# Kernel optimization log

Hardware: AMD Instinct MI355X
Metric: run time of the kernel (lower is better)

The kernel has to match this reference:

```python
import jax, jax.numpy as jnp
import numpy as np

B, L, HS, WS = 4, 5, 32, 32
C = 256            # dim == heads * dim_head
M, D = 8, 32       # heads, dim_head
T, R = 2, 4        # num_types, num_relations
I = M * D          # inner_dim
EPS = 1e-5


def setup_inputs() -> dict:
    key = jax.random.key(0)
    ks = jax.random.split(key, 12)
    w = 0.02
    x = jax.random.normal(ks[0], (B, L, HS, WS, C), dtype=jnp.float32)
    mask = jnp.ones((B, HS, WS, L, L), dtype=jnp.int32)
    prior_encoding = jax.random.randint(ks[1], (B, L, HS, WS, 3), 0, T).astype(jnp.float32)
    return {
        "x": x,
        "mask": mask,
        "prior_encoding": prior_encoding,
        "ln_w": jnp.ones((C,), jnp.float32),
        "ln_b": jnp.zeros((C,), jnp.float32),
        "Wq": jax.random.normal(ks[2], (T, C, I), jnp.float32) * w,
        "bq": jnp.zeros((T, I), jnp.float32),
        "Wk": jax.random.normal(ks[3], (T, C, I), jnp.float32) * w,
        "bk": jnp.zeros((T, I), jnp.float32),
        "Wv": jax.random.normal(ks[4], (T, C, I), jnp.float32) * w,
        "bv": jnp.zeros((T, I), jnp.float32),
        "Wa": jax.random.normal(ks[5], (T, I, C), jnp.float32) * w,
        "ba": jnp.zeros((T, C), jnp.float32),
        "rel_att": jax.random.normal(ks[6], (R, M, D, D), jnp.float32) * w,
        "rel_msg": jax.random.normal(ks[7], (R, M, D, D), jnp.float32) * w,
    }


def _hgt_forward(x, mask, prior_encoding, ln_w, ln_b, Wq, bq, Wk, bk, Wv, bv, Wa, ba, rel_att, rel_msg):
    # pre-LayerNorm over channel dim
    mu = jnp.mean(x, axis=-1, keepdims=True)
    var = jnp.mean(jnp.square(x - mu), axis=-1, keepdims=True)
    xn = (x - mu) * jax.lax.rsqrt(var + EPS) * ln_w + ln_b

    # [B,L,H,W,C] -> [B,H,W,L,C]
    xp = jnp.transpose(xn, (0, 2, 3, 1, 4))
    types = prior_encoding[:, :, 0, 0, 2].astype(jnp.int32)  # [B,L]

    # per-type q/k/v projections via gather of type-indexed weights
    q = jnp.einsum('bhwlc,blci->bhwli', xp, Wq[types]) + bq[types][:, None, None]
    k = jnp.einsum('bhwlc,blci->bhwli', xp, Wk[types]) + bk[types][:, None, None]
    v = jnp.einsum('bhwlc,blci->bhwli', xp, Wv[types]) + bv[types][:, None, None]

    def to_heads(t):  # [B,H,W,L,I] -> [B,M,H,W,L,D]
        return jnp.transpose(t.reshape(B, HS, WS, L, M, D), (0, 4, 1, 2, 3, 5))
    q, k, v = to_heads(q), to_heads(k), to_heads(v)

    # relation-indexed edge weights: e_type = t_i * T + t_j
    e = types[:, :, None] * T + types[:, None, :]              # [B,L,L]
    w_att = jnp.transpose(rel_att[e], (0, 3, 1, 2, 4, 5))      # [B,M,L,L,D,D]
    w_msg = jnp.transpose(rel_msg[e], (0, 3, 1, 2, 4, 5))

    scale = D ** -0.5
    q_w = jnp.einsum('bmhwip,bmijpq->bmhwijq', q, w_att)
    att = jnp.einsum('bmhwijq,bmhwjq->bmhwij', q_w, k) * scale
    att = jnp.where(mask[:, None] == 0, -1e9, att)
    att = jax.nn.softmax(att, axis=-1)

    v_msg = jnp.einsum('bmijpc,bmhwjp->bmhwijc', w_msg, v)
    out = jnp.einsum('bmhwij,bmhwijc->bmhwic', att, v_msg)

    # [B,M,H,W,L,D] -> [B,H,W,L,C]
    out = jnp.transpose(out, (0, 2, 3, 4, 1, 5)).reshape(B, HS, WS, L, I)
    out = jnp.einsum('bhwli,blic->bhwlc', out, Wa[types]) + ba[types][:, None, None]
    # dropout is identity at inference
    return jnp.transpose(out, (0, 3, 1, 2, 4))                 # [B,L,H,W,C]


def reference(x, mask, prior_encoding, ln_w, ln_b, Wq, bq, Wk, bk, Wv, bv, Wa, ba, rel_att, rel_msg):
    return _hgt_forward(x, mask, prior_encoding, ln_w, ln_b, Wq, bq, Wk, bk, Wv, bv, Wa, ba, rel_att, rel_msg)
```

## Files before the change

### kernel.cpp

```cpp
#include <hip/hip_runtime.h>
#include <hip/hip_bf16.h>
#include <math.h>

#define BB 4
#define LL 5
#define HSZ 32
#define WSZ 32
#define PP (HSZ*WSZ)
#define CC 256
#define MM 8
#define DD 32
#define II 256
#define TT 2
#define NTOK (BB*PP*LL*II)
#define TILE_ELEMS 8192
#define SCALE 0.17677669529663687f

typedef short bf16x8 __attribute__((ext_vector_type(8)));
typedef float f32x4 __attribute__((ext_vector_type(4)));

static __device__ __forceinline__ ushort f2bf(float f) {
    unsigned u = __float_as_uint(f);
    unsigned r = (u + 0x7fffu + ((u >> 16) & 1u)) >> 16;
    return (ushort)r;
}
static __device__ __forceinline__ float bf2f(ushort u) {
    return __uint_as_float(((unsigned)u) << 16);
}

__global__ __launch_bounds__(256) void k_fold(
    const float* __restrict__ Wq, const float* __restrict__ Wv,
    const float* __restrict__ Wk, const float* __restrict__ Wa,
    const float* __restrict__ bq, const float* __restrict__ bv,
    const float* __restrict__ rel_att, const float* __restrict__ rel_msg,
    const float* __restrict__ x,
    const float* __restrict__ lnw, const float* __restrict__ lnb,
    ushort* __restrict__ packW, float* __restrict__ bEff,
    ushort* __restrict__ xnPack)
{
    __shared__ float As[1024];
    __shared__ ushort Apack[8192];
    const int blk = blockIdx.x;
    const int tid = threadIdx.x;

    if (blk < 64) {
        const int p  = blk >> 5;
        const int t  = (blk >> 4) & 1;
        const int ts = (blk >> 3) & 1;
        const int m  = blk & 7;
        const float* A = (p == 0)
            ? rel_att + (size_t)((t * 2 + ts) * 8 + m) * 1024
            : rel_msg + (size_t)((ts * 2 + t) * 8 + m) * 1024;
        for (int i = tid; i < 1024; i += 256) As[i] = A[i];
        __syncthreads();

        const float* W = ((p == 0) ? Wq : Wv) + (size_t)t * 65536;
        const int k = tid;
        float wrow[32];
        #pragma unroll
        for (int u = 0; u < 8; ++u)
            *(float4*)&wrow[u * 4] = *(const float4*)&W[k * 256 + m * 32 + u * 4];

        const int slot = (p == 0 ? 0 : 4) + t * 2 + ts;
        ushort* base = packW + (size_t)slot * 65536;
        const int kt = k >> 5, j = k & 7, lq = ((k >> 3) & 3) * 16;
        #pragma unroll
        for (int q = 0; q < 32; ++q) {
            float acc = 0.f;
            #pragma unroll
            for (int pp = 0; pp < 32; ++pp) acc += wrow[pp] * As[pp * 32 + q];
            const int nt = m * 2 + (q >> 4);
            const int lane = lq + (q & 15);
            base[(size_t)((nt * 8 + kt) * 64 + lane) * 8 + j] = f2bf(acc);
        }
        if (tid < 32) {
            const int q = tid;
            const float* bi = ((p == 0) ? bq : bv) + t * 256 + m * 32;
            float acc = 0.f;
            #pragma unroll
            for (int pp = 0; pp < 32; ++pp) acc += bi[pp] * As[pp * 32 + q];
            bEff[(p ? 1024 : 0) + (t * 2 + ts) * 256 + m * 32 + q] = acc;
        }
    } else if (blk < 192) {
        const int idx = blk - 64;
        const int which = idx >> 6;
        const int gi = (idx & 63) * 256 + tid;
        const int t = gi >> 13;
        const int sub = gi & 8191;
        const float* src = ((which == 0) ? Wk : Wa) + (size_t)t * 65536;
        const int slot = (which == 0 ? 8 : 10) + t;
        const int nt = sub >> 9, kt = (sub >> 6) & 7, lane = sub & 63;
        const int k0 = kt * 32 + (lane >> 4) * 8;
        const int n  = nt * 16 + (lane & 15);
        ushort h[8];
        #pragma unroll
        for (int j = 0; j < 8; ++j) h[j] = f2bf(src[(size_t)(k0 + j) * 256 + n]);
        uint4 o;
        o.x = (unsigned)h[0] | ((unsigned)h[1] << 16);
        o.y = (unsigned)h[2] | ((unsigned)h[3] << 16);
        o.z = (unsigned)h[4] | ((unsigned)h[5] << 16);
        o.w = (unsigned)h[6] | ((unsigned)h[7] << 16);
        *(uint4*)(packW + (size_t)slot * 65536 + (size_t)sub * 8) = o;
    } else {
        const int lblk = blk - 192;
        const int bl  = lblk >> 5;
        const int pt  = lblk & 31;
        const int p0  = pt * 32;

        const int r  = tid >> 3;
        const int jj = tid & 7;
        const float* xrow = x + ((size_t)bl * PP + p0 + r) * CC;
        float4 xv[8];
        float s1 = 0.f, s2 = 0.f;
        #pragma unroll
        for (int u = 0; u < 8; ++u) {
            xv[u] = *(const float4*)(xrow + jj * 32 + u * 4);
            s1 += xv[u].x + xv[u].y + xv[u].z + xv[u].w;
            s2 += xv[u].x * xv[u].x + xv[u].y * xv[u].y + xv[u].z * xv[u].z + xv[u].w * xv[u].w;
        }
        s1 += __shfl_xor(s1, 1); s1 += __shfl_xor(s1, 2); s1 += __shfl_xor(s1, 4);
        s2 += __shfl_xor(s2, 1); s2 += __shfl_xor(s2, 2); s2 += __shfl_xor(s2, 4);
        const float mu   = s1 * (1.0f / 256.0f);
        const float var  = s2 * (1.0f / 256.0f) - mu * mu;
        const float rstd = rsqrtf(var + 1e-5f);

        const int mt_r = r >> 4, rm = r & 15;
        #pragma unroll
        for (int u = 0; u < 8; ++u) {
            const int c0 = jj * 32 + u * 4;
            const float4 g  = *(const float4*)(lnw + c0);
            const float4 bt = *(const float4*)(lnb + c0);
            const ushort h0 = f2bf((xv[u].x - mu) * rstd * g.x + bt.x);
            const ushort h1 = f2bf((xv[u].y - mu) * rstd * g.y + bt.y);
            const ushort h2 = f2bf((xv[u].z - mu) * rstd * g.z + bt.z);
            const ushort h3 = f2bf((xv[u].w - mu) * rstd * g.w + bt.w);
            uint2 w2;
            w2.x = (unsigned)h0 | ((unsigned)h1 << 16);
            w2.y = (unsigned)h2 | ((unsigned)h3 << 16);
            const int kt   = c0 >> 5;
            const int lsub = rm + (((c0 >> 3) & 3) << 4);
            const int j0   = c0 & 7;
            *(uint2*)&Apack[(((mt_r * 8 + kt) * 64 + lsub) << 3) + j0] = w2;
        }
        __syncthreads();

        const size_t tbase = (size_t)lblk * TILE_ELEMS;
        #pragma unroll
        for (int u = 0; u < 4; ++u) {
            const int ch = (tid + u * 256) * 8;
            *(uint4*)&xnPack[tbase + ch] = *(const uint4*)&Apack[ch];
        }
    }
}

__global__ __launch_bounds__(256) void k_proj(
    const ushort* __restrict__ xnPack, const float* __restrict__ prior,
    const ushort* __restrict__ packW, const float* __restrict__ bEff,
    const float* __restrict__ bk,
    ushort* __restrict__ qw0, ushort* __restrict__ qw1, ushort* __restrict__ kkO,
    ushort* __restrict__ vm0, ushort* __restrict__ vm1)
{
    __shared__ ushort As[8192];

    const int tid  = threadIdx.x;
    const int blk  = blockIdx.x;
    const int mat  = blk / 640;
    const int rem  = blk - mat * 640;
    const int bl   = rem >> 5;
    const int sub  = rem & 31;
    const int pg   = sub >> 1;
    const int half = sub & 1;
    const int t    = (int)prior[(size_t)bl * (PP * 3) + 2];

    int slot; const float* bias;
    if (mat < 2)       { slot = t * 2 + mat;           bias = bEff + slot * 256; }
    else if (mat == 2) { slot = 8 + t;                 bias = bk + t * 256; }
    else               { slot = 4 + t * 2 + (mat - 3); bias = bEff + 1024 + (t * 2 + (mat - 3)) * 256; }
    ushort* dst = (mat == 0) ? qw0 : (mat == 1) ? qw1 : (mat == 2) ? kkO : (mat == 3) ? vm0 : vm1;

    const int wv = tid >> 6, lane = tid & 63;

    const ushort* Bp = packW + (size_t)slot * 65536;
    bf16x8 bfr[8][2];
    #pragma unroll
    for (int kt = 0; kt < 8; ++kt)
        #pragma unroll
        for (int nn = 0; nn < 2; ++nn) {
            const int ntg = half * 8 + wv * 2 + nn;
            bfr[kt][nn] = *(const bf16x8*)&Bp[(size_t)((ntg * 8 + kt) * 64 + lane) * 8];
        }

    const int cl = lane & 15, rq = lane >> 4;
    const int colA = half * 128 + wv * 32 + cl;
    const int colB = colA + 16;
    const float biasA = bias[colA], biasB = bias[colB];

    #pragma unroll 1
    for (int tl = 0; tl < 2; ++tl) {
        const int pt = pg * 2 + tl;
        const size_t tbase = (size_t)(bl * 32 + pt) * TILE_ELEMS;
        __syncthreads();
        #pragma unroll
        for (int u = 0; u < 4; ++u) {
            const int ch = (tid + u * 256) * 8;
            *(uint4*)&As[ch] = *(const uint4*)&xnPack[tbase + ch];
        }
        __syncthreads();

        f32x4 acc[2][2];
        #pragma unroll
        for (int mt = 0; mt < 2; ++mt)
            #pragma unroll
            for (int nn = 0; nn < 2; ++nn)
                acc[mt][nn] = (f32x4){0.f, 0.f, 0.f, 0.f};

        #pragma unroll
        for (int kt = 0; kt < 8; ++kt) {
            const bf16x8 a0 = *(const bf16x8*)&As[((0 * 8 + kt) * 64 + lane) << 3];
            const bf16x8 a1 = *(const bf16x8*)&As[((1 * 8 + kt) * 64 + lane) << 3];
            acc[0][0] = __builtin_amdgcn_mfma_f32_16x16x32_bf16(a0, bfr[kt][0], acc[0][0], 0, 0, 0);
            acc[0][1] = __builtin_amdgcn_mfma_f32_16x16x32_bf16(a0, bfr[kt][1], acc[0][1], 0, 0, 0);
            acc[1][0] = __builtin_amdgcn_mfma_f32_16x16x32_bf16(a1, bfr[kt][0], acc[1][0], 0, 0, 0);
            acc[1][1] = __builtin_amdgcn_mfma_f32_16x16x32_bf16(a1, bfr[kt][1], acc[1][1], 0, 0, 0);
        }

        const int p0 = pt * 32;
        #pragma unroll
        for (int mt = 0; mt < 2; ++mt) {
            const int row0 = p0 + mt * 16 + rq * 4;
            #pragma unroll
            for (int r2 = 0; r2 < 4; ++r2) {
                const size_t rb = ((size_t)bl * PP + row0 + r2) * II;
                dst[rb + colA] = f2bf(acc[mt][0][r2] + biasA);
                dst[rb + colB] = f2bf(acc[mt][1][r2] + biasB);
            }
        }
    }
}

__global__ __launch_bounds__(256) void k_attn(
    const ushort* __restrict__ qw0, const ushort* __restrict__ qw1,
    const ushort* __restrict__ kkI,
    const ushort* __restrict__ vm0, const ushort* __restrict__ vm1,
    const int* __restrict__ mask, const float* __restrict__ prior,
    ushort* __restrict__ ao)
{
    const int tid  = threadIdx.x;
    const int site = blockIdx.x * 4 + (tid >> 6);
    const int lane = tid & 63;
    const int b    = site >> 10;
    const int pix  = site & 1023;
    const int c0   = lane * 4;

    const int usite = __builtin_amdgcn_readfirstlane(site);
    const int ub    = usite >> 10;

    int ty[5];
    #pragma unroll
    for (int l = 0; l < 5; ++l)
        ty[l] = (int)prior[(size_t)(ub * 5 + l) * (PP * 3) + 2];

    int mv[5][5];
    #pragma unroll
    for (int i = 0; i < 5; ++i)
        #pragma unroll
        for (int j = 0; j < 5; ++j)
            mv[i][j] = mask[(size_t)usite * 25 + i * 5 + j];

    float qf[2][5][4], kf[5][4];
    #pragma unroll
    for (int l = 0; l < 5; ++l) {
        const size_t base = (((size_t)(b * 5 + l) << 10) + pix) * II + c0;
        const ushort4 q0 = *(const ushort4*)(qw0 + base);
        const ushort4 q1 = *(const ushort4*)(qw1 + base);
        const ushort4 kv = *(const ushort4*)(kkI + base);
        qf[0][l][0] = bf2f(q0.x); qf[0][l][1] = bf2f(q0.y); qf[0][l][2] = bf2f(q0.z); qf[0][l][3] = bf2f(q0.w);
        qf[1][l][0] = bf2f(q1.x); qf[1][l][1] = bf2f(q1.y); qf[1][l][2] = bf2f(q1.z); qf[1][l][3] = bf2f(q1.w);
        kf[l][0]    = bf2f(kv.x); kf[l][1]    = bf2f(kv.y); kf[l][2]    = bf2f(kv.z); kf[l][3]    = bf2f(kv.w);
    }

    float s[5][5];
    #pragma unroll
    for (int j = 0; j < 5; ++j) {
        if (ty[j]) {
            #pragma unroll
            for (int i = 0; i < 5; ++i)
                s[i][j] = qf[1][i][0] * kf[j][0] + qf[1][i][1] * kf[j][1]
                        + qf[1][i][2] * kf[j][2] + qf[1][i][3] * kf[j][3];
        } else {
            #pragma unroll
            for (int i = 0; i < 5; ++i)
                s[i][j] = qf[0][i][0] * kf[j][0] + qf[0][i][1] * kf[j][1]
                        + qf[0][i][2] * kf[j][2] + qf[0][i][3] * kf[j][3];
        }
    }
    #pragma unroll
    for (int i = 0; i < 5; ++i)
        #pragma unroll
        for (int j = 0; j < 5; ++j) s[i][j] += __shfl_xor(s[i][j], 1);
    #pragma unroll
    for (int i = 0; i < 5; ++i)
        #pragma unroll
        for (int j = 0; j < 5; ++j) s[i][j] += __shfl_xor(s[i][j], 2);
    #pragma unroll
    for (int i = 0; i < 5; ++i)
        #pragma unroll
        for (int j = 0; j < 5; ++j) s[i][j] += __shfl_xor(s[i][j], 4);

    float vf[2][5][4];
    #pragma unroll
    for (int l = 0; l < 5; ++l) {
        const size_t base = (((size_t)(b * 5 + l) << 10) + pix) * II + c0;
        const ushort4 v0 = *(const ushort4*)(vm0 + base);
        const ushort4 v1 = *(const ushort4*)(vm1 + base);
        vf[0][l][0] = bf2f(v0.x); vf[0][l][1] = bf2f(v0.y); vf[0][l][2] = bf2f(v0.z); vf[0][l][3] = bf2f(v0.w);
        vf[1][l][0] = bf2f(v1.x); vf[1][l][1] = bf2f(v1.y); vf[1][l][2] = bf2f(v1.z); vf[1][l][3] = bf2f(v1.w);
    }

    #pragma unroll
    for (int i = 0; i < 5; ++i) {
        float lg[5];
        #pragma unroll
        for (int j = 0; j < 5; ++j)
            lg[j] = mv[i][j] ? s[i][j] * SCALE : -1e9f;
        const float mx = fmaxf(fmaxf(fmaxf(lg[0], lg[1]), fmaxf(lg[2], lg[3])), lg[4]);
        float ex[5], sum = 0.f;
        #pragma unroll
        for (int j = 0; j < 5; ++j) { ex[j] = __expf(lg[j] - mx); sum += ex[j]; }
        const float rs = 1.0f / sum;
        float o0 = 0.f, o1 = 0.f, o2 = 0.f, o3 = 0.f;
        if (ty[i]) {
            #pragma unroll
            for (int j = 0; j < 5; ++j) {
                o0 += ex[j] * vf[1][j][0]; o1 += ex[j] * vf[1][j][1];
                o2 += ex[j] * vf[1][j][2]; o3 += ex[j] * vf[1][j][3];
            }
        } else {
            #pragma unroll
            for (int j = 0; j < 5; ++j) {
                o0 += ex[j] * vf[0][j][0]; o1 += ex[j] * vf[0][j][1];
                o2 += ex[j] * vf[0][j][2]; o3 += ex[j] * vf[0][j][3];
            }
        }
        o0 *= rs; o1 *= rs; o2 *= rs; o3 *= rs;
        uint2 w2;
        w2.x = (unsigned)f2bf(o0) | ((unsigned)f2bf(o1) << 16);
        w2.y = (unsigned)f2bf(o2) | ((unsigned)f2bf(o3) << 16);
        *(uint2*)&ao[(((size_t)(b * 5 + i) << 10) + pix) * II + c0] = w2;
    }
}

__global__ __launch_bounds__(256) void k_out(
    const ushort* __restrict__ ao, const float* __restrict__ prior,
    const ushort* __restrict__ packW, const float* __restrict__ ba,
    float* __restrict__ out)
{
    __shared__ float obufF[32 * 132];

    const int tid  = threadIdx.x;
    const int blk  = blockIdx.x;
    const int bl   = blk >> 6;
    const int sub  = blk & 63;
    const int pt   = sub >> 1;
    const int half = sub & 1;
    const int bbi  = bl / LL;
    const int l    = bl - bbi * LL;
    const int t    = (int)prior[(size_t)bl * (PP * 3) + 2];

    const int wv = tid >> 6, lane = tid & 63;
    const ushort* Bp = packW + (size_t)(10 + t) * 65536;
    bf16x8 bfr[8][2];
    #pragma unroll
    for (int kt = 0; kt < 8; ++kt)
        #pragma unroll
        for (int nn = 0; nn < 2; ++nn) {
            const int ntg = half * 8 + wv * 2 + nn;
            bfr[kt][nn] = *(const bf16x8*)&Bp[(size_t)((ntg * 8 + kt) * 64 + lane) * 8];
        }

    const int p0   = pt * 32;
    const int rowA = lane & 15;
    const int ksub = (lane >> 4) * 8;
    const ushort* a_base = ao + ((size_t)(bl * PP + p0 + rowA)) * II + ksub;

    const int cl = lane & 15, rq = lane >> 4;
    const int colL_A = wv * 32 + cl;
    const int colL_B = colL_A + 16;
    const float biasA = ba[t * CC + half * 128 + colL_A];
    const float biasB = ba[t * CC + half * 128 + colL_B];

    f32x4 acc[2][2];
    #pragma unroll
    for (int mt = 0; mt < 2; ++mt)
        #pragma unroll
        for (int nn = 0; nn < 2; ++nn)
            acc[mt][nn] = (f32x4){0.f, 0.f, 0.f, 0.f};

    #pragma unroll
    for (int kt = 0; kt < 8; ++kt) {
        const bf16x8 a0 = *(const bf16x8*)(a_base + kt * 32);
        const bf16x8 a1 = *(const bf16x8*)(a_base + (size_t)16 * II + kt * 32);
        acc[0][0] = __builtin_amdgcn_mfma_f32_16x16x32_bf16(a0, bfr[kt][0], acc[0][0], 0, 0, 0);
        acc[0][1] = __builtin_amdgcn_mfma_f32_16x16x32_bf16(a0, bfr[kt][1], acc[0][1], 0, 0, 0);
        acc[1][0] = __builtin_amdgcn_mfma_f32_16x16x32_bf16(a1, bfr[kt][0], acc[1][0], 0, 0, 0);
        acc[1][1] = __builtin_amdgcn_mfma_f32_16x16x32_bf16(a1, bfr[kt][1], acc[1][1], 0, 0, 0);
    }

    #pragma unroll
    for (int mt = 0; mt < 2; ++mt) {
        const int rowb = mt * 16 + rq * 4;
        #pragma unroll
        for (int r2 = 0; r2 < 4; ++r2) {
            obufF[(rowb + r2) * 132 + colL_A] = acc[mt][0][r2] + biasA;
            obufF[(rowb + r2) * 132 + colL_B] = acc[mt][1][r2] + biasB;
        }
    }
    __syncthreads();

    #pragma unroll
    for (int k2 = 0; k2 < 4; ++k2) {
        const int id  = tid + k2 * 256;
        const int row = id >> 5;
        const int ch  = (id & 31) * 4;
        const float4 v4 = *(const float4*)&obufF[row * 132 + ch];
        *(float4*)(out + ((size_t)(bbi * LL + l) * PP + p0 + row) * CC + half * 128 + ch) = v4;
    }
}

extern "C" void kernel_launch(void* const* d_in, const int* in_sizes, int n_in,
                              void* d_out, int out_size, void* d_ws, size_t ws_size,
                              hipStream_t stream) {
    const float* x       = (const float*)d_in[0];
    const int*   mask    = (const int*)d_in[1];
    const float* prior   = (const float*)d_in[2];
    const float* lnw     = (const float*)d_in[3];
    const float* lnb     = (const float*)d_in[4];
    const float* Wq      = (const float*)d_in[5];
    const float* bq      = (const float*)d_in[6];
    const float* Wk      = (const float*)d_in[7];
    const float* bk      = (const float*)d_in[8];
    const float* Wv      = (const float*)d_in[9];
    const float* bv      = (const float*)d_in[10];
    const float* Wa      = (const float*)d_in[11];
    const float* ba      = (const float*)d_in[12];
    const float* rel_att = (const float*)d_in[13];
    const float* rel_msg = (const float*)d_in[14];
    float* out = (float*)d_out;

    ushort* qw0    = (ushort*)d_ws;
    ushort* qw1    = qw0 + NTOK;
    ushort* kko    = qw1 + NTOK;
    ushort* vm0    = kko + NTOK;
    ushort* vm1    = vm0 + NTOK;
    ushort* ao     = vm1 + NTOK;
    ushort* xnPack = ao + NTOK;
    ushort* packW  = xnPack + NTOK;
    float*  bEff   = (float*)(packW + 12 * 65536);

    hipLaunchKernelGGL(k_fold, dim3(832), dim3(256), 0, stream,
                       Wq, Wv, Wk, Wa, bq, bv, rel_att, rel_msg,
                       x, lnw, lnb, packW, bEff, xnPack);
    hipLaunchKernelGGL(k_proj, dim3(3200), dim3(256), 0, stream,
                       xnPack, prior, packW, bEff, bk, qw0, qw1, kko, vm0, vm1);
    hipLaunchKernelGGL(k_attn, dim3(1024), dim3(256), 0, stream,
                       qw0, qw1, kko, vm0, vm1, mask, prior, ao);
    hipLaunchKernelGGL(k_out, dim3(1280), dim3(256), 0, stream,
                       ao, prior, packW, ba, out);
}
```

Measured before the change: 154.9 us.

## Fuse attention and output projection kernels via shared-memory staging

Merges the attention kernel and the output projection GEMM into a single kernel. Each block computes attention for 16 pixels across all 5 layers and stages the bf16 result in LDS, then runs the MFMA output projection per layer straight from LDS. This removes the global write and re-read of the attention output buffer and one kernel launch. In exchange the grid shrinks to 512 blocks, which limits parallelism. Every block (each half) also recomputes the full attention, duplicating that work, and reloads the weight fragments once per layer.

```diff
diff --git a/kernel.cpp b/kernel.cpp
--- a/kernel.cpp
+++ b/kernel.cpp
@@ -238,192 +238,180 @@
     }
 }
 
-__global__ __launch_bounds__(256) void k_attn(
+__global__ __launch_bounds__(256) void k_attn_out(
     const ushort* __restrict__ qw0, const ushort* __restrict__ qw1,
     const ushort* __restrict__ kkI,
     const ushort* __restrict__ vm0, const ushort* __restrict__ vm1,
     const int* __restrict__ mask, const float* __restrict__ prior,
-    ushort* __restrict__ ao)
+    const ushort* __restrict__ packW, const float* __restrict__ ba,
+    float* __restrict__ out)
 {
+    __shared__ ushort aoS[5 * 16 * 264];
+    __shared__ float obufF[16 * 132];
+
     const int tid  = threadIdx.x;
-    const int site = blockIdx.x * 4 + (tid >> 6);
-    const int lane = tid & 63;
-    const int b    = site >> 10;
-    const int pix  = site & 1023;
+    const int blk  = blockIdx.x;
+    const int half = blk & 1;
+    const int gg   = blk >> 1;
+    const int b    = gg >> 6;
+    const int pg   = gg & 63;
+    const int p0   = pg * 16;
+    const int wv   = tid >> 6, lane = tid & 63;
     const int c0   = lane * 4;
-
-    const int usite = __builtin_amdgcn_readfirstlane(site);
-    const int ub    = usite >> 10;
 
     int ty[5];
     #pragma unroll
     for (int l = 0; l < 5; ++l)
-        ty[l] = (int)prior[(size_t)(ub * 5 + l) * (PP * 3) + 2];
-
-    int mv[5][5];
-    #pragma unroll
-    for (int i = 0; i < 5; ++i)
-        #pragma unroll
-        for (int j = 0; j < 5; ++j)
-            mv[i][j] = mask[(size_t)usite * 25 + i * 5 + j];
-
-    float qf[2][5][4], kf[5][4];
-    #pragma unroll
-    for (int l = 0; l < 5; ++l) {
-        const size_t base = (((size_t)(b * 5 + l) << 10) + pix) * II + c0;
-        const ushort4 q0 = *(const ushort4*)(qw0 + base);
-        const ushort4 q1 = *(const ushort4*)(qw1 + base);
-        const ushort4 kv = *(const ushort4*)(kkI + base);
-        qf[0][l][0] = bf2f(q0.x); qf[0][l][1] = bf2f(q0.y); qf[0][l][2] = bf2f(q0.z); qf[0][l][3] = bf2f(q0.w);
-        qf[1][l][0] = bf2f(q1.x); qf[1][l][1] = bf2f(q1.y); qf[1][l][2] = bf2f(q1.z); qf[1][l][3] = bf2f(q1.w);
-        kf[l][0]    = bf2f(kv.x); kf[l][1]    = bf2f(kv.y); kf[l][2]    = bf2f(kv.z); kf[l][3]    = bf2f(kv.w);
+        ty[l] = (int)prior[(size_t)(b * 5 + l) * (PP * 3) + 2];
+
+    #pragma unroll 1
+    for (int it = 0; it < 4; ++it) {
+        const int sl   = wv * 4 + it;
+        const int pix  = p0 + sl;
+        const int site = b * 1024 + pix;
+        const int usite = __builtin_amdgcn_readfirstlane(site);
+
+        int mv[5][5];
+        #pragma unroll
+        for (int i = 0; i < 5; ++i)
+            #pragma unroll
+            for (int j = 0; j < 5; ++j)
+                mv[i][j] = mask[(size_t)usite * 25 + i * 5 + j];
+
+        float qf[2][5][4], kf[5][4];
+        #pragma unroll
+        for (int l = 0; l < 5; ++l) {
+            const size_t base = (((size_t)(b * 5 + l) << 10) + pix) * II + c0;
+            const ushort4 q0 = *(const ushort4*)(qw0 + base);
+            const ushort4 q1 = *(const ushort4*)(qw1 + base);
+            const ushort4 kv = *(const ushort4*)(kkI + base);
+            qf[0][l][0] = bf2f(q0.x); qf[0][l][1] = bf2f(q0.y); qf[0][l][2] = bf2f(q0.z); qf[0][l][3] = bf2f(q0.w);
+            qf[1][l][0] = bf2f(q1.x); qf[1][l][1] = bf2f(q1.y); qf[1][l][2] = bf2f(q1.z); qf[1][l][3] = bf2f(q1.w);
+            kf[l][0]    = bf2f(kv.x); kf[l][1]    = bf2f(kv.y); kf[l][2]    = bf2f(kv.z); kf[l][3]    = bf2f(kv.w);
+        }
+
+        float s[5][5];
+        #pragma unroll
+        for (int j = 0; j < 5; ++j) {
+            if (ty[j]) {
+                #pragma unroll
+                for (int i = 0; i < 5; ++i)
+                    s[i][j] = qf[1][i][0] * kf[j][0] + qf[1][i][1] * kf[j][1]
+                            + qf[1][i][2] * kf[j][2] + qf[1][i][3] * kf[j][3];
+            } else {
+                #pragma unroll
+                for (int i = 0; i < 5; ++i)
+                    s[i][j] = qf[0][i][0] * kf[j][0] + qf[0][i][1] * kf[j][1]
+                            + qf[0][i][2] * kf[j][2] + qf[0][i][3] * kf[j][3];
+            }
+        }
+        #pragma unroll
+        for (int i = 0; i < 5; ++i)
+            #pragma unroll
+            for (int j = 0; j < 5; ++j) s[i][j] += __shfl_xor(s[i][j], 1);
+        #pragma unroll
+        for (int i = 0; i < 5; ++i)
+            #pragma unroll
+            for (int j = 0; j < 5; ++j) s[i][j] += __shfl_xor(s[i][j], 2);
+        #pragma unroll
+        for (int i = 0; i < 5; ++i)
+            #pragma unroll
+            for (int j = 0; j < 5; ++j) s[i][j] += __shfl_xor(s[i][j], 4);
+
+        float vf[2][5][4];
+        #pragma unroll
+        for (int l = 0; l < 5; ++l) {
+            const size_t base = (((size_t)(b * 5 + l) << 10) + pix) * II + c0;
+            const ushort4 v0 = *(const ushort4*)(vm0 + base);
+            const ushort4 v1 = *(const ushort4*)(vm1 + base);
+            vf[0][l][0] = bf2f(v0.x); vf[0][l][1] = bf2f(v0.y); vf[0][l][2] = bf2f(v0.z); vf[0][l][3] = bf2f(v0.w);
+            vf[1][l][0] = bf2f(v1.x); vf[1][l][1] = bf2f(v1.y); vf[1][l][2] = bf2f(v1.z); vf[1][l][3] = bf2f(v1.w);
+        }
+
+        #pragma unroll
+        for (int i = 0; i < 5; ++i) {
+            float lg[5];
+            #pragma unroll
+            for (int j = 0; j < 5; ++j)
+                lg[j] = mv[i][j] ? s[i][j] * SCALE : -1e9f;
+            const float mx = fmaxf(fmaxf(fmaxf(lg[0], lg[1]), fmaxf(lg[2], lg[3])), lg[4]);
+            float ex[5], sum = 0.f;
+            #pragma unroll
+            for (int j = 0; j < 5; ++j) { ex[j] = __expf(lg[j] - mx); sum += ex[j]; }
+            const float rs = 1.0f / sum;
+            float o0 = 0.f, o1 = 0.f, o2 = 0.f, o3 = 0.f;
+            if (ty[i]) {
+                #pragma unroll
+                for (int j = 0; j < 5; ++j) {
+                    o0 += ex[j] * vf[1][j][0]; o1 += ex[j] * vf[1][j][1];
+                    o2 += ex[j] * vf[1][j][2]; o3 += ex[j] * vf[1][j][3];
+                }
+            } else {
+                #pragma unroll
+                for (int j = 0; j < 5; ++j) {
+                    o0 += ex[j] * vf[0][j][0]; o1 += ex[j] * vf[0][j][1];
+                    o2 += ex[j] * vf[0][j][2]; o3 += ex[j] * vf[0][j][3];
+                }
+            }
+            o0 *= rs; o1 *= rs; o2 *= rs; o3 *= rs;
+            uint2 w2;
+            w2.x = (unsigned)f2bf(o0) | ((unsigned)f2bf(o1) << 16);
+            w2.y = (unsigned)f2bf(o2) | ((unsigned)f2bf(o3) << 16);
+            *(uint2*)&aoS[(i * 16 + sl) * 264 + c0] = w2;
+        }
     }
-
-    float s[5][5];
-    #pragma unroll
-    for (int j = 0; j < 5; ++j) {
-        if (ty[j]) {
-            #pragma unroll
-            for (int i = 0; i < 5; ++i)
-                s[i][j] = qf[1][i][0] * kf[j][0] + qf[1][i][1] * kf[j][1]
-                        + qf[1][i][2] * kf[j][2] + qf[1][i][3] * kf[j][3];
-        } else {
-            #pragma unroll
-            for (int i = 0; i < 5; ++i)
-                s[i][j] = qf[0][i][0] * kf[j][0] + qf[0][i][1] * kf[j][1]
-                        + qf[0][i][2] * kf[j][2] + qf[0][i][3] * kf[j][3];
-        }
-    }
-    #pragma unroll
-    for (int i = 0; i < 5; ++i)
-        #pragma unroll
-        for (int j = 0; j < 5; ++j) s[i][j] += __shfl_xor(s[i][j], 1);
-    #pragma unroll
-    for (int i = 0; i < 5; ++i)
-        #pragma unroll
-        for (int j = 0; j < 5; ++j) s[i][j] += __shfl_xor(s[i][j], 2);
-    #pragma unroll
-    for (int i = 0; i < 5; ++i)
-        #pragma unroll
-        for (int j = 0; j < 5; ++j) s[i][j] += __shfl_xor(s[i][j], 4);
-
-    float vf[2][5][4];
-    #pragma unroll
-    for (int l = 0; l < 5; ++l) {
-        const size_t base = (((size_t)(b * 5 + l) << 10) + pix) * II + c0;
-        const ushort4 v0 = *(const ushort4*)(vm0 + base);
-        const ushort4 v1 = *(const ushort4*)(vm1 + base);
-        vf[0][l][0] = bf2f(v0.x); vf[0][l][1] = bf2f(v0.y); vf[0][l][2] = bf2f(v0.z); vf[0][l][3] = bf2f(v0.w);
-        vf[1][l][0] = bf2f(v1.x); vf[1][l][1] = bf2f(v1.y); vf[1][l][2] = bf2f(v1.z); vf[1][l][3] = bf2f(v1.w);
-    }
-
-    #pragma unroll
-    for (int i = 0; i < 5; ++i) {
-        float lg[5];
-        #pragma unroll
-        for (int j = 0; j < 5; ++j)
-            lg[j] = mv[i][j] ? s[i][j] * SCALE : -1e9f;
-        const float mx = fmaxf(fmaxf(fmaxf(lg[0], lg[1]), fmaxf(lg[2], lg[3])), lg[4]);
-        float ex[5], sum = 0.f;
-        #pragma unroll
-        for (int j = 0; j < 5; ++j) { ex[j] = __expf(lg[j] - mx); sum += ex[j]; }
-        const float rs = 1.0f / sum;
-        float o0 = 0.f, o1 = 0.f, o2 = 0.f, o3 = 0.f;
-        if (ty[i]) {
-            #pragma unroll
-            for (int j = 0; j < 5; ++j) {
-                o0 += ex[j] * vf[1][j][0]; o1 += ex[j] * vf[1][j][1];
-                o2 += ex[j] * vf[1][j][2]; o3 += ex[j] * vf[1][j][3];
-            }
-        } else {
-            #pragma unroll
-            for (int j = 0; j < 5; ++j) {
-                o0 += ex[j] * vf[0][j][0]; o1 += ex[j] * vf[0][j][1];
-                o2 += ex[j] * vf[0][j][2]; o3 += ex[j] * vf[0][j][3];
-            }
-        }
-        o0 *= rs; o1 *= rs; o2 *= rs; o3 *= rs;
-        uint2 w2;
-        w2.x = (unsigned)f2bf(o0) | ((unsigned)f2bf(o1) << 16);
-        w2.y = (unsigned)f2bf(o2) | ((unsigned)f2bf(o3) << 16);
-        *(uint2*)&ao[(((size_t)(b * 5 + i) << 10) + pix) * II + c0] = w2;
-    }
-}
-
-__global__ __launch_bounds__(256) void k_out(
-    const ushort* __restrict__ ao, const float* __restrict__ prior,
-    const ushort* __restrict__ packW, const float* __restrict__ ba,
-    float* __restrict__ out)
-{
-    __shared__ float obufF[32 * 132];
-
-    const int tid  = threadIdx.x;
-    const int blk  = blockIdx.x;
-    const int bl   = blk >> 6;
-    const int sub  = blk & 63;
-    const int pt   = sub >> 1;
-    const int half = sub & 1;
-    const int bbi  = bl / LL;
-    const int l    = bl - bbi * LL;
-    const int t    = (int)prior[(size_t)bl * (PP * 3) + 2];
-
-    const int wv = tid >> 6, lane = tid & 63;
-    const ushort* Bp = packW + (size_t)(10 + t) * 65536;
-    bf16x8 bfr[8][2];
-    #pragma unroll
-    for (int kt = 0; kt < 8; ++kt)
-        #pragma unroll
-        for (int nn = 0; nn < 2; ++nn) {
-            const int ntg = half * 8 + wv * 2 + nn;
-            bfr[kt][nn] = *(const bf16x8*)&Bp[(size_t)((ntg * 8 + kt) * 64 + lane) * 8];
-        }
-
-    const int p0   = pt * 32;
+    __syncthreads();
+
+    const int cl = lane & 15, rq = lane >> 4;
     const int rowA = lane & 15;
     const int ksub = (lane >> 4) * 8;
-    const ushort* a_base = ao + ((size_t)(bl * PP + p0 + rowA)) * II + ksub;
-
-    const int cl = lane & 15, rq = lane >> 4;
     const int colL_A = wv * 32 + cl;
     const int colL_B = colL_A + 16;
-    const float biasA = ba[t * CC + half * 128 + colL_A];
-    const float biasB = ba[t * CC + half * 128 + colL_B];
-
-    f32x4 acc[2][2];
-    #pragma unroll
-    for (int mt = 0; mt < 2; ++mt)
-        #pragma unroll
-        for (int nn = 0; nn < 2; ++nn)
-            acc[mt][nn] = (f32x4){0.f, 0.f, 0.f, 0.f};
-
-    #pragma unroll
-    for (int kt = 0; kt < 8; ++kt) {
-        const bf16x8 a0 = *(const bf16x8*)(a_base + kt * 32);
-        const bf16x8 a1 = *(const bf16x8*)(a_base + (size_t)16 * II + kt * 32);
-        acc[0][0] = __builtin_amdgcn_mfma_f32_16x16x32_bf16(a0, bfr[kt][0], acc[0][0], 0, 0, 0);
-        acc[0][1] = __builtin_amdgcn_mfma_f32_16x16x32_bf16(a0, bfr[kt][1], acc[0][1], 0, 0, 0);
-        acc[1][0] = __builtin_amdgcn_mfma_f32_16x16x32_bf16(a1, bfr[kt][0], acc[1][0], 0, 0, 0);
-        acc[1][1] = __builtin_amdgcn_mfma_f32_16x16x32_bf16(a1, bfr[kt][1], acc[1][1], 0, 0, 0);
-    }
-
-    #pragma unroll
-    for (int mt = 0; mt < 2; ++mt) {
-        const int rowb = mt * 16 + rq * 4;
+
+    #pragma unroll 1
+    for (int l = 0; l < 5; ++l) {
+        const int t = ty[l];
+        const ushort* Bp = packW + (size_t)(10 + t) * 65536;
+        bf16x8 bfr[8][2];
+        #pragma unroll
+        for (int kt = 0; kt < 8; ++kt)
+            #pragma unroll
+            for (int nn = 0; nn < 2; ++nn) {
+                const int ntg = half * 8 + wv * 2 + nn;
+                bfr[kt][nn] = *(const bf16x8*)&Bp[(size_t)((ntg * 8 + kt) * 64 + lane) * 8];
+            }
+
+        f32x4 acc[2];
+        acc[0] = (f32x4){0.f, 0.f, 0.f, 0.f};
+        acc[1] = (f32x4){0.f, 0.f, 0.f, 0.f};
+
+        const ushort* aRow = &aoS[(l * 16 + rowA) * 264 + ksub];
+        #pragma unroll
+        for (int kt = 0; kt < 8; ++kt) {
+            const bf16x8 a0 = *(const bf16x8*)(aRow + kt * 32);
+            acc[0] = __builtin_amdgcn_mfma_f32_16x16x32_bf16(a0, bfr[kt][0], acc[0], 0, 0, 0);
+            acc[1] = __builtin_amdgcn_mfma_f32_16x16x32_bf16(a0, bfr[kt][1], acc[1], 0, 0, 0);
+        }
+
+        const float biasA = ba[t * CC + half * 128 + colL_A];
+        const float biasB = ba[t * CC + half * 128 + colL_B];
+
+        __syncthreads();
         #pragma unroll
         for (int r2 = 0; r2 < 4; ++r2) {
-            obufF[(rowb + r2) * 132 + colL_A] = acc[mt][0][r2] + biasA;
-            obufF[(rowb + r2) * 132 + colL_B] = acc[mt][1][r2] + biasB;
-        }
-    }
-    __syncthreads();
-
-    #pragma unroll
-    for (int k2 = 0; k2 < 4; ++k2) {
-        const int id  = tid + k2 * 256;
-        const int row = id >> 5;
-        const int ch  = (id & 31) * 4;
-        const float4 v4 = *(const float4*)&obufF[row * 132 + ch];
-        *(float4*)(out + ((size_t)(bbi * LL + l) * PP + p0 + row) * CC + half * 128 + ch) = v4;
+            obufF[(rq * 4 + r2) * 132 + colL_A] = acc[0][r2] + biasA;
+            obufF[(rq * 4 + r2) * 132 + colL_B] = acc[1][r2] + biasB;
+        }
+        __syncthreads();
+
+        #pragma unroll
+        for (int k2 = 0; k2 < 2; ++k2) {
+            const int id  = tid + k2 * 256;
+            const int row = id >> 5;
+            const int ch  = (id & 31) * 4;
+            const float4 v4 = *(const float4*)&obufF[row * 132 + ch];
+            *(float4*)(out + ((size_t)(b * LL + l) * PP + p0 + row) * CC + half * 128 + ch) = v4;
+        }
     }
 }
 
@@ -452,8 +440,7 @@
     ushort* kko    = qw1 + NTOK;
     ushort* vm0    = kko + NTOK;
     ushort* vm1    = vm0 + NTOK;
-    ushort* ao     = vm1 + NTOK;
-    ushort* xnPack = ao + NTOK;
+    ushort* xnPack = vm1 + NTOK;
     ushort* packW  = xnPack + NTOK;
     float*  bEff   = (float*)(packW + 12 * 65536);
 
@@ -462,8 +449,6 @@
                        x, lnw, lnb, packW, bEff, xnPack);
     hipLaunchKernelGGL(k_proj, dim3(3200), dim3(256), 0, stream,
                        xnPack, prior, packW, bEff, bk, qw0, qw1, kko, vm0, vm1);
-    hipLaunchKernelGGL(k_attn, dim3(1024), dim3(256), 0, stream,
-                       qw0, qw1, kko, vm0, vm1, mask, prior, ao);
-    hipLaunchKernelGGL(k_out, dim3(1280), dim3(256), 0, stream,
-                       ao, prior, packW, ba, out);
-}
+    hipLaunchKernelGGL(k_attn_out, dim3(512), dim3(256), 0, stream,
+                       qw0, qw1, kko, vm0, vm1, mask, prior, packW, ba, out);
+}
```

Measured after the change: 159.1 us. 2.7% more time.
